# Kernel tuning notes

Hardware: AMD Instinct MI355X
Metric: run time of the kernel (lower is better)

Reference implementation:

```python
import jax, jax.numpy as jnp
import numpy as np


def setup_inputs() -> dict:
    key = jax.random.key(0)
    k1, k2, k3, k4, k5 = jax.random.split(key, 5)
    B, S, IC, OC = 4, 2048, 4096, 4096
    n_out = int(0.05 * IC)  # 204 outlier columns
    return {
        "x": jax.random.normal(k1, (B, S, IC), dtype=jnp.float32),
        "weight": jax.random.normal(k2, (OC, IC), dtype=jnp.float32) * 0.02,
        "bias": jax.random.normal(k3, (OC,), dtype=jnp.float32) * 0.02,
        "outlier_weight": jax.random.normal(k4, (OC, n_out), dtype=jnp.float32) * 0.02,
        "outlier_columns_index": jax.random.randint(k5, (n_out,), 0, IC, dtype=jnp.int32),
    }


def reference(x, weight, bias, outlier_weight, outlier_columns_index):
    # XnorBinaryLinear.quant_weight: per-output-row mean-centering,
    # sign binarization, scaled by per-row mean absolute value.
    mean = jnp.mean(weight, axis=1, keepdims=True)            # [OC, 1]
    centered = weight - mean                                  # [OC, IC]
    scale = jnp.mean(jnp.abs(centered), axis=1, keepdims=True)  # [OC, 1]
    q = jnp.sign(centered) * scale                            # binarized weight [OC, IC]
    # scatter fp32 outlier columns back into the binarized weight
    w = q.at[:, outlier_columns_index].set(outlier_weight)    # [OC, IC]
    # F.linear(x, w, bias) = x @ w.T + bias
    out = jnp.einsum('bsi,oi->bso', x, w) + bias
    return out
```

## Files before the change

kernel.cpp:

```cpp
#include <hip/hip_runtime.h>
#include <hip/hip_bf16.h>


typedef __attribute__((ext_vector_type(4))) int i32x4;

__global__ void init_colmap_kernel(int* __restrict__ cm, int IC) {
    int i = blockIdx.x * 256 + threadIdx.x;
    if (i < IC) cm[i] = -1;
}

__global__ void scatter_colmap_kernel(const int* __restrict__ idx,
                                      int* __restrict__ cm, int n) {
    int j = blockIdx.x * 256 + threadIdx.x;
    if (j < n) atomicMax(&cm[idx[j]], j);
}

__global__ void quant_sign_kernel(const float* __restrict__ w,
                                  const float* __restrict__ ow,
                                  const int* __restrict__ idx,
                                  const int* __restrict__ cm,
                                  signed char* __restrict__ qw,
                                  float* __restrict__ sArr,
                                  int IC, int K2, int n_out) {
    __shared__ float red[8];
    __shared__ signed char sgn[4096];
    const int o = blockIdx.x;
    const int t = threadIdx.x;
    const int lane = t & 63, wid = t >> 6;

    const float4* row4 = (const float4*)(w + (size_t)o * IC);
    float4 v[4];
    float s = 0.f;
#pragma unroll
    for (int j = 0; j < 4; ++j) {
        v[j] = row4[t + j * 256];
        s += v[j].x + v[j].y + v[j].z + v[j].w;
    }
#pragma unroll
    for (int off = 32; off; off >>= 1) s += __shfl_down(s, off);
    if (lane == 0) red[wid] = s;
    __syncthreads();
    const float mean = (red[0] + red[1] + red[2] + red[3]) / (float)IC;

    float a = 0.f;
#pragma unroll
    for (int j = 0; j < 4; ++j)
        a += fabsf(v[j].x - mean) + fabsf(v[j].y - mean) +
             fabsf(v[j].z - mean) + fabsf(v[j].w - mean);
#pragma unroll
    for (int off = 32; off; off >>= 1) a += __shfl_down(a, off);
    if (lane == 0) red[4 + wid] = a;
    __syncthreads();
    const float scale = (red[4] + red[5] + red[6] + red[7]) / (float)IC;
    if (t == 0) sArr[o] = scale;

    const size_t base = (size_t)o * K2;
#pragma unroll
    for (int j = 0; j < 4; ++j) {
        const int c0 = (t + j * 256) * 4;
        float ee[4] = {v[j].x, v[j].y, v[j].z, v[j].w};
        int pack = 0;
#pragma unroll
        for (int ei = 0; ei < 4; ++ei) {
            float c = ee[ei] - mean;
            int q = c > 0.f ? 8 : (c < 0.f ? -8 : 0);
            pack |= (q & 0xff) << (ei * 8);
        }
        *(int*)(qw + base + c0) = pack;
        *(int*)(sgn + c0) = pack;
    }
    __syncthreads();

    signed char q = 0;
    if (t < n_out) {
        const int c = idx[t];
        if (cm[c] == t) {
            const float sg = (float)sgn[c] * 0.125f;
            const float wc = ow[(size_t)o * n_out + t] - scale * sg;
            float qf = rintf(8.f * wc / scale);
            qf = fminf(127.f, fmaxf(-127.f, qf));
            q = (signed char)(int)qf;
        }
    }
    qw[base + IC + t] = q;
}

__global__ void quant_x_kernel(const float4* __restrict__ x4,
                               const int* __restrict__ idx,
                               signed char* __restrict__ qx,
                               float* __restrict__ rdel,
                               int IC, int K2, int n_out) {
    __shared__ float red[4];
    __shared__ float bmax;
    __shared__ signed char rowq[4096];
    const int m = blockIdx.x;
    const int t = threadIdx.x;
    const int lane = t & 63, wid = t >> 6;

    const float4* row4 = x4 + (size_t)m * (IC / 4);
    float4 v[4];
    float mx = 0.f;
#pragma unroll
    for (int j = 0; j < 4; ++j) {
        v[j] = row4[t + j * 256];
        mx = fmaxf(mx, fmaxf(fmaxf(fabsf(v[j].x), fabsf(v[j].y)),
                             fmaxf(fabsf(v[j].z), fabsf(v[j].w))));
    }
#pragma unroll
    for (int off = 32; off; off >>= 1) mx = fmaxf(mx, __shfl_down(mx, off));
    if (lane == 0) red[wid] = mx;
    __syncthreads();
    if (t == 0) {
        float m0 = fmaxf(fmaxf(red[0], red[1]), fmaxf(red[2], red[3]));
        bmax = m0;
        rdel[m] = m0 / 127.f;
    }
    __syncthreads();
    const float inv = 127.f / bmax;

    const size_t base = (size_t)m * K2;
#pragma unroll
    for (int j = 0; j < 4; ++j) {
        const int c0 = (t + j * 256) * 4;
        float ee[4] = {v[j].x, v[j].y, v[j].z, v[j].w};
        int pack = 0;
#pragma unroll
        for (int ei = 0; ei < 4; ++ei) {
            int q = (int)rintf(ee[ei] * inv);
            pack |= (q & 0xff) << (ei * 8);
        }
        *(int*)(qx + base + c0) = pack;
        *(int*)(rowq + c0) = pack;
    }
    __syncthreads();

    signed char g = 0;
    if (t < n_out) g = rowq[idx[t]];
    qx[base + IC + t] = g;
}

#define GLDS(src, dst) __builtin_amdgcn_global_load_lds( \
    (const __attribute__((address_space(1))) void*)(src), \
    (__attribute__((address_space(3))) void*)(dst), 16, 0, 0)

#define STAGE64(MAT, bufS, knB) do {                                          \
    const signed char* gsrc_ = (MAT) ? Bblk : Ablk;                           \
    _Pragma("unroll")                                                         \
    for (int rr_ = 0; rr_ < 2; ++rr_) {                                       \
      GLDS(gsrc_ + (size_t)(rr_ * 128 + stg_row) * K2 + (knB) + stg_col,      \
           &ldsb[(bufS) * 32768 + (MAT) * 16384 + (rr_ * 128 + wid * 16) * 64]); \
    } } while (0)

#define RDA(AF, FH, B_) do {                                                  \
    const signed char* pa_ = &ldsb[(B_) * 32768];                             \
    _Pragma("unroll")                                                         \
    for (int j_ = 0; j_ < 4; ++j_)                                            \
      AF[j_] = *(const i32x4*)&pa_[(wr * 128 + ((FH) * 4 + j_) * 16 + l15) * 64 + slB]; \
  } while (0)

#define RDB(BF, B_) do {                                                      \
    const signed char* pb_ = &ldsb[(B_) * 32768 + 16384];                     \
    _Pragma("unroll")                                                         \
    for (int j_ = 0; j_ < 4; ++j_)                                            \
      BF[j_] = *(const i32x4*)&pb_[(wc * 64 + j_ * 16 + l15) * 64 + slB];     \
  } while (0)

#define MM16(FH) do {                                                         \
    _Pragma("unroll")                                                         \
    for (int mi_ = 0; mi_ < 4; ++mi_)                                         \
      _Pragma("unroll")                                                       \
      for (int ni_ = 0; ni_ < 4; ++ni_)                                       \
        acc[(FH) * 4 + mi_][ni_] = __builtin_amdgcn_mfma_i32_16x16x64_i8(     \
            afr[mi_], bfr[ni_], acc[(FH) * 4 + mi_][ni_], 0, 0, 0);           \
  } while (0)

#define PH64(FH, DOBF, STMAT, VM, bufR, bufS, knB) do {                       \
    if (DOBF) RDB(bfr, bufR);                                                 \
    RDA(afr, FH, bufR);                                                       \
    STAGE64(STMAT, bufS, knB);                                                \
    if (VM) asm volatile("s_waitcnt vmcnt(8)" ::: "memory");                  \
    __builtin_amdgcn_s_barrier();                                             \
    __builtin_amdgcn_s_setprio(1);                                            \
    MM16(FH);                                                                 \
    __builtin_amdgcn_s_setprio(0);                                            \
    __builtin_amdgcn_s_barrier();                                             \
  } while (0)

#define KT64(bufR, bufS, knB) do {                                            \
    PH64(0, true,  0, false, bufR, bufS, knB);                                \
    PH64(1, false, 1, true,  bufR, bufS, knB);                                \
  } while (0)

__global__ __launch_bounds__(512, 2) void gemm_i8_kernel(
    const signed char* __restrict__ Aq,
    const signed char* __restrict__ Bq,
    const float* __restrict__ bias,
    const float* __restrict__ sArr,
    const float* __restrict__ rdel,
    float* __restrict__ C,
    int M, int N, int K2, int NBN) {
    extern __shared__ signed char ldsb[];

    const int t = threadIdx.x;
    const int wid = t >> 6, lane = t & 63;
    const int l15 = lane & 15;
    const int slB = (((lane >> 4) ^ ((lane >> 1) & 3)) & 3) * 16;
    const int wr = wid >> 2;
    const int wc = wid & 3;
    const int stg_row = wid * 16 + (lane >> 2);
    const int stg_col = (((lane & 3) ^ ((lane >> 3) & 3)) & 3) * 16;

    const int nwg = gridDim.x;
    const int bid = blockIdx.x;
    const int q = nwg >> 3, r = nwg & 7;
    const int xcd = bid & 7, off = bid >> 3;
    const int swz = (xcd < r ? xcd * (q + 1) : r * (q + 1) + (xcd - r) * q) + off;
    const int bm = swz / NBN, bn = swz % NBN;

    const signed char* Ablk = Aq + (size_t)(bm * 256) * K2;
    const signed char* Bblk = Bq + (size_t)(bn * 256) * K2;

    i32x4 acc[8][4] = {};
    i32x4 afr[4], bfr[4];

    STAGE64(0, 0, 0);    STAGE64(1, 0, 0);
    STAGE64(0, 1, 64);   STAGE64(1, 1, 64);
    STAGE64(0, 2, 128);  STAGE64(1, 2, 128);
    asm volatile("s_waitcnt vmcnt(8)" ::: "memory");
    __builtin_amdgcn_s_barrier();

    for (int it = 0; it < 17; ++it) {
        const int tt = it * 4;
        const int k3 = (tt + 3) * 64;
        const int k4 = (tt + 4 < 68) ? (tt + 4) * 64 : 0;
        const int k5 = (tt + 5 < 68) ? (tt + 5) * 64 : 0;
        const int k6 = (tt + 6 < 68) ? (tt + 6) * 64 : 0;
        KT64(0, 3, k3);
        KT64(1, 0, k4);
        KT64(2, 1, k5);
        KT64(3, 2, k6);
    }

    float sv[4], bv[4];
#pragma unroll
    for (int ni = 0; ni < 4; ++ni) {
        const int col = bn * 256 + wc * 64 + ni * 16 + l15;
        sv[ni] = sArr[col] * 0.125f;
        bv[ni] = bias[col];
    }

    const int crow0 = bm * 256 + wr * 128;
    const int ccol = bn * 256 + wc * 64 + l15;
#pragma unroll
    for (int mi = 0; mi < 8; ++mi) {
#pragma unroll
        for (int rr = 0; rr < 4; ++rr) {
            const int row = crow0 + mi * 16 + (lane >> 4) * 4 + rr;
            const float rd = rdel[row];
            float* Crow = C + (size_t)row * N;
#pragma unroll
            for (int ni = 0; ni < 4; ++ni)
                Crow[ccol + ni * 16] =
                    (float)acc[mi][ni][rr] * (sv[ni] * rd) + bv[ni];
        }
    }
}

extern "C" void kernel_launch(void* const* d_in, const int* in_sizes, int n_in,
                              void* d_out, int out_size, void* d_ws, size_t ws_size,
                              hipStream_t stream) {
    const float* x      = (const float*)d_in[0];
    const float* weight = (const float*)d_in[1];
    const float* bias   = (const float*)d_in[2];
    const float* ow     = (const float*)d_in[3];
    const int*   idx    = (const int*)d_in[4];

    const int OC    = in_sizes[2];
    const int n_out = in_sizes[4];
    const int IC    = in_sizes[1] / OC;
    const int M     = in_sizes[0] / IC;
    const int K2    = IC + 256;
    float* out = (float*)d_out;

    char* ws = (char*)d_ws;
    signed char* qx = (signed char*)ws;
    signed char* qw = (signed char*)(ws + (size_t)M * K2);
    float* sArr = (float*)(ws + (size_t)M * K2 + (size_t)OC * K2);
    float* rdel = sArr + OC;
    int*   cm   = (int*)(rdel + M);

    init_colmap_kernel<<<(IC + 255) / 256, 256, 0, stream>>>(cm, IC);
    scatter_colmap_kernel<<<(n_out + 255) / 256, 256, 0, stream>>>(idx, cm, n_out);
    quant_sign_kernel<<<OC, 256, 0, stream>>>(weight, ow, idx, cm, qw, sArr,
                                              IC, K2, n_out);
    quant_x_kernel<<<M, 256, 0, stream>>>((const float4*)x, idx, qx, rdel,
                                          IC, K2, n_out);

    hipFuncSetAttribute((const void*)gemm_i8_kernel,
                        hipFuncAttributeMaxDynamicSharedMemorySize, 131072);
    const int NBM = M / 256, NBN = OC / 256;
    gemm_i8_kernel<<<dim3(NBM * NBN), dim3(512), 131072, stream>>>(
        qx, qw, bias, sArr, rdel, out, M, OC, K2, NBN);
}
```

Before: 188.7 us.

## Fold column-map build into quant kernel and drop mid-tile GEMM barriers

Two kernel launches that built a global outlier column map are removed. Each quant_sign block now builds its own map in shared memory using LDS atomics. In the GEMM K-loop, the barrier pair around the first half-tile MFMA phase is removed, so the first 16 MFMAs run without waiting on other waves. This saves launch overhead and synchronisation. The cost is redundant per-block map construction, and the LDS hazards between staging and reading become harder to reason about.

New measurement: 179.5 us. 1.05x faster.

```diff
diff --git a/kernel.cpp b/kernel.cpp
--- a/kernel.cpp
+++ b/kernel.cpp
@@ -3,31 +3,23 @@
 
 
 typedef __attribute__((ext_vector_type(4))) int i32x4;
-
-__global__ void init_colmap_kernel(int* __restrict__ cm, int IC) {
-    int i = blockIdx.x * 256 + threadIdx.x;
-    if (i < IC) cm[i] = -1;
-}
-
-__global__ void scatter_colmap_kernel(const int* __restrict__ idx,
-                                      int* __restrict__ cm, int n) {
-    int j = blockIdx.x * 256 + threadIdx.x;
-    if (j < n) atomicMax(&cm[idx[j]], j);
-}
 
 __global__ void quant_sign_kernel(const float* __restrict__ w,
                                   const float* __restrict__ ow,
                                   const int* __restrict__ idx,
-                                  const int* __restrict__ cm,
                                   signed char* __restrict__ qw,
                                   float* __restrict__ sArr,
                                   int IC, int K2, int n_out) {
     __shared__ float red[8];
     __shared__ signed char sgn[4096];
+    __shared__ int cmL[4096];
     const int o = blockIdx.x;
     const int t = threadIdx.x;
     const int lane = t & 63, wid = t >> 6;
 
+#pragma unroll
+    for (int i = 0; i < 16; ++i) cmL[t + i * 256] = -1;
+
     const float4* row4 = (const float4*)(w + (size_t)o * IC);
     float4 v[4];
     float s = 0.f;
@@ -41,6 +33,8 @@
     if (lane == 0) red[wid] = s;
     __syncthreads();
     const float mean = (red[0] + red[1] + red[2] + red[3]) / (float)IC;
+
+    if (t < n_out) atomicMax(&cmL[idx[t]], t);
 
     float a = 0.f;
 #pragma unroll
@@ -74,7 +68,7 @@
     signed char q = 0;
     if (t < n_out) {
         const int c = idx[t];
-        if (cm[c] == t) {
+        if (cmL[c] == t) {
             const float sg = (float)sgn[c] * 0.125f;
             const float wc = ow[(size_t)o * n_out + t] - scale * sg;
             float qf = rintf(8.f * wc / scale);
@@ -174,21 +168,21 @@
             afr[mi_], bfr[ni_], acc[(FH) * 4 + mi_][ni_], 0, 0, 0);           \
   } while (0)
 
-#define PH64(FH, DOBF, STMAT, VM, bufR, bufS, knB) do {                       \
-    if (DOBF) RDB(bfr, bufR);                                                 \
-    RDA(afr, FH, bufR);                                                       \
-    STAGE64(STMAT, bufS, knB);                                                \
-    if (VM) asm volatile("s_waitcnt vmcnt(8)" ::: "memory");                  \
+#define KT64(bufR, bufS, knB) do {                                            \
+    RDB(bfr, bufR);                                                           \
+    RDA(afr, 0, bufR);                                                        \
+    STAGE64(0, bufS, knB);                                                    \
+    __builtin_amdgcn_s_setprio(1);                                            \
+    MM16(0);                                                                  \
+    __builtin_amdgcn_s_setprio(0);                                            \
+    RDA(afr, 1, bufR);                                                        \
+    STAGE64(1, bufS, knB);                                                    \
+    asm volatile("s_waitcnt vmcnt(8)" ::: "memory");                          \
     __builtin_amdgcn_s_barrier();                                             \
     __builtin_amdgcn_s_setprio(1);                                            \
-    MM16(FH);                                                                 \
+    MM16(1);                                                                  \
     __builtin_amdgcn_s_setprio(0);                                            \
     __builtin_amdgcn_s_barrier();                                             \
-  } while (0)
-
-#define KT64(bufR, bufS, knB) do {                                            \
-    PH64(0, true,  0, false, bufR, bufS, knB);                                \
-    PH64(1, false, 1, true,  bufR, bufS, knB);                                \
   } while (0)
 
 __global__ __launch_bounds__(512, 2) void gemm_i8_kernel(
@@ -287,11 +281,8 @@
     signed char* qw = (signed char*)(ws + (size_t)M * K2);
     float* sArr = (float*)(ws + (size_t)M * K2 + (size_t)OC * K2);
     float* rdel = sArr + OC;
-    int*   cm   = (int*)(rdel + M);
-
-    init_colmap_kernel<<<(IC + 255) / 256, 256, 0, stream>>>(cm, IC);
-    scatter_colmap_kernel<<<(n_out + 255) / 256, 256, 0, stream>>>(idx, cm, n_out);
-    quant_sign_kernel<<<OC, 256, 0, stream>>>(weight, ow, idx, cm, qw, sArr,
+
+    quant_sign_kernel<<<OC, 256, 0, stream>>>(weight, ow, idx, qw, sArr,
                                               IC, K2, n_out);
     quant_x_kernel<<<M, 256, 0, stream>>>((const float4*)x, idx, qx, rdel,
                                           IC, K2, n_out);
```
